# Kernel optimization log

Measured on AMD Instinct MI355X. Metric: run time of the kernel, lower is better.

## Reference

```python
import jax, jax.numpy as jnp
import numpy as np

B, V, H, NT, K_CD = 4096, 1024, 1024, 2, 10
L1_REG, L2_REG = 1e-5, 1e-4


def setup_inputs() -> dict:
    key = jax.random.key(0)
    ks = jax.random.split(key, 10)
    v0 = jax.random.bernoulli(ks[0], 0.5, (B, V)).astype(jnp.float32)
    # two distinct non-trivial (non-Z) sites per sample, one in each half
    tau0 = jax.random.randint(ks[1], (B,), 0, V // 2)
    tau1 = V // 2 + jax.random.randint(ks[2], (B,), 0, V // 2)
    tau_idx = jnp.stack([tau0, tau1], axis=1).astype(jnp.int32)
    basis_choice = jax.random.randint(ks[3], (B, NT), 1, 3).astype(jnp.int32)  # X=1 or Y=2
    basis_ids = jnp.zeros((B, V), jnp.int32)
    basis_ids = basis_ids.at[jnp.arange(B)[:, None], tau_idx].set(basis_choice)
    s = 1.0 / np.sqrt(2.0)
    un = np.zeros((3, 2, 2, 2), np.float32)  # [basis, row, col, re/im]
    un[0, :, :, 0] = np.eye(2)                              # Z: identity
    un[1, :, :, 0] = s * np.array([[1, 1], [1, -1]])        # X: Hadamard
    un[2, :, :, 0] = s * np.array([[1, 0], [1, 0]])         # Y: K gate, real
    un[2, :, :, 1] = s * np.array([[0, -1], [0, 1]])        # Y: K gate, imag
    unitaries = jnp.asarray(un)
    weights_amp = jax.random.normal(ks[4], (H, V), jnp.float32) / np.sqrt(V)
    weights_phase = 0.01 * jax.random.normal(ks[5], (H, V), jnp.float32)
    visible_bias_amp = 0.01 * jax.random.normal(ks[6], (V,), jnp.float32)
    hidden_bias_amp = 0.01 * jax.random.normal(ks[7], (H,), jnp.float32)
    visible_bias_phase = 0.01 * jax.random.normal(ks[8], (V,), jnp.float32)
    hidden_bias_phase = 0.01 * jax.random.normal(ks[9], (H,), jnp.float32)
    return {"v0": v0, "basis_ids": basis_ids, "tau_idx": tau_idx, "unitaries": unitaries,
            "weights_amp": weights_amp, "visible_bias_amp": visible_bias_amp,
            "hidden_bias_amp": hidden_bias_amp, "weights_phase": weights_phase,
            "visible_bias_phase": visible_bias_phase, "hidden_bias_phase": hidden_bias_phase,
            "k": K_CD}


def _forward(v0, unitaries, weights_amp, visible_bias_amp, hidden_bias_amp,
             weights_phase, visible_bias_phase, hidden_bias_phase,
             basis_ids, tau_idx, k):
    Bsz, Vn = v0.shape
    NTn = tau_idx.shape[1]
    C = 2 ** NTn
    # all 2^NT assignments of the rotated (tau) sites -> [C, NT]
    S = jnp.asarray(np.array([[(c >> (NTn - 1 - t)) & 1 for t in range(NTn)]
                              for c in range(C)], np.int32))
    U = (unitaries[..., 0] + 1j * unitaries[..., 1]).astype(jnp.complex64)  # [3,2,2]
    b_tau = jnp.take_along_axis(basis_ids, tau_idx, axis=1)                 # [B,NT]
    v0_tau = jnp.take_along_axis(v0, tau_idx, axis=1).astype(jnp.int32)     # [B,NT]
    # product over tau sites of unitary elements U_b[v0_j, s_j] -> [B,C]
    Uelem = U[b_tau[:, None, :], v0_tau[:, None, :], S[None, :, :]]
    wU = jnp.prod(Uelem, axis=-1)
    # v' = v0 with tau sites replaced by each assignment s -> [B,C,V]
    onehot = jax.nn.one_hot(tau_idx, Vn, dtype=v0.dtype)                    # [B,NT,V]
    mask = onehot.sum(1)
    vp = v0[:, None, :] * (1.0 - mask[:, None, :]) \
         + jnp.einsum('btv,ct->bcv', onehot, S.astype(v0.dtype))
    # unnormalized wavefunction psi(v') = sqrt(p_amp(v')) * exp(i*log(p_phase(v'))/2)
    pre_amp = jnp.einsum('bcv,hv->bch', vp, weights_amp) + hidden_bias_amp
    pre_ph = jnp.einsum('bcv,hv->bch', vp, weights_phase) + hidden_bias_phase
    log_amp = 0.5 * (vp @ visible_bias_amp + jax.nn.softplus(pre_amp).sum(-1))  # [B,C]
    theta = 0.5 * (vp @ visible_bias_phase + jax.nn.softplus(pre_ph).sum(-1))
    # per-sample shift cancels exactly in A/B; keeps exp() in fp32 range
    log_amp = log_amp - jax.lax.stop_gradient(log_amp.max(axis=1, keepdims=True))
    psi = (jnp.exp(log_amp) * (jnp.cos(theta) + 1j * jnp.sin(theta))).astype(jnp.complex64)
    w = wU * psi                                   # [B,C] complex
    coef = w / w.sum(axis=1, keepdims=True)        # A/B weighting per sample
    sig_amp = jax.nn.sigmoid(pre_amp)
    sig_ph = jax.nn.sigmoid(pre_ph)
    inv_b = 1.0 / Bsz
    Lw_amp = jnp.einsum('bc,bch,bcv->hv', coef, sig_amp, vp) * inv_b
    Lw_ph = jnp.einsum('bc,bch,bcv->hv', coef, sig_ph, vp) * inv_b
    Lvb = jnp.einsum('bc,bcv->v', coef, vp) * inv_b
    Lhb_amp = jnp.einsum('bc,bch->h', coef, sig_amp) * inv_b
    Lhb_ph = jnp.einsum('bc,bch->h', coef, sig_ph) * inv_b
    # amplitude params take Re(L) (negated positive phase); phase params take Im(L)
    g_w_amp = -jnp.real(Lw_amp)
    g_vb_amp = -jnp.real(Lvb)
    g_hb_amp = -jnp.real(Lhb_amp)
    g_w_ph = jnp.imag(Lw_ph)
    g_vb_ph = jnp.imag(Lvb)
    g_hb_ph = jnp.imag(Lhb_ph)
    # ---- CD-k Gibbs negative phase (amplitude RBM only) ----
    base_key = jax.random.key(1234)
    def gibbs_step(i, v):
        kh = jax.random.fold_in(base_key, 2 * i)
        kv = jax.random.fold_in(base_key, 2 * i + 1)
        ph = jax.nn.sigmoid(v @ weights_amp.T + hidden_bias_amp)
        h = (jax.random.uniform(kh, ph.shape) < ph).astype(v.dtype)
        pv = jax.nn.sigmoid(h @ weights_amp + visible_bias_amp)
        return (jax.random.uniform(kv, pv.shape) < pv).astype(v.dtype)
    vk = jax.lax.stop_gradient(jax.lax.fori_loop(0, k, gibbs_step, v0))
    sig_k = jax.nn.sigmoid(vk @ weights_amp.T + hidden_bias_amp)
    g_w_amp = g_w_amp + jnp.einsum('bh,bv->hv', sig_k, vk) * inv_b
    g_vb_amp = g_vb_amp + vk.mean(0)
    g_hb_amp = g_hb_amp + sig_k.mean(0)
    # ---- L1/L2 regularization on weight gradients ----
    g_w_amp = g_w_amp + L2_REG * weights_amp + L1_REG * jnp.sign(weights_amp)
    g_w_ph = g_w_ph + L2_REG * weights_phase + L1_REG * jnp.sign(weights_phase)
    return (g_w_amp, g_vb_amp, g_hb_amp, g_w_ph, g_vb_ph, g_hb_ph)


def reference(v0, basis_ids, tau_idx, unitaries, weights_amp, visible_bias_amp,
              hidden_bias_amp, weights_phase, visible_bias_phase, hidden_bias_phase, k):
    return _forward(v0, unitaries, weights_amp, visible_bias_amp, hidden_bias_amp,
                    weights_phase, visible_bias_phase, hidden_bias_phase,
                    basis_ids, tau_idx, k)
```

## Files before the change

kernel.cpp:

```cpp
#include <hip/hip_runtime.h>
#include <cstdint>
#include <cstddef>

#define BSZ 4096
#define VN  1024
#define HN  1024
#define NSTEPS 10

static constexpr float INVB = 1.0f / 4096.0f;
static constexpr float L1R  = 1e-5f;
static constexpr float L2R  = 1e-4f;

typedef __attribute__((ext_vector_type(8)))  __bf16        bf16x8;
typedef __attribute__((ext_vector_type(8)))  unsigned short ushort8;
typedef __attribute__((ext_vector_type(16))) float          f32x16;

__device__ static inline unsigned short f2bf(float x){
  unsigned u = __float_as_uint(x);
  unsigned r = (u + 0x7FFFu + ((u >> 16) & 1u)) >> 16;
  return (unsigned short)r;
}
__device__ static inline float bf2f(unsigned short s){
  return __uint_as_float(((unsigned)s) << 16);
}

__device__ __forceinline__ void gload16(const void* g, void* l){
  __builtin_amdgcn_global_load_lds(
      (__attribute__((address_space(1))) void*)(g),
      (__attribute__((address_space(3))) void*)(l),
      16, 0, 0);
}

#define TFR(x0,x1,r) { x0 += x1; x1 = ((x1)<<(r))|((x1)>>(32-(r))); x1 ^= x0; }

__host__ __device__ static inline void tf2x32(unsigned k0, unsigned k1,
                                              unsigned x0, unsigned x1,
                                              unsigned &o0, unsigned &o1)
{
  const unsigned ks2 = k0 ^ k1 ^ 0x1BD11BDAu;
  x0 += k0; x1 += k1;
  TFR(x0,x1,13) TFR(x0,x1,15) TFR(x0,x1,26) TFR(x0,x1,6)
  x0 += k1; x1 += ks2 + 1u;
  TFR(x0,x1,17) TFR(x0,x1,29) TFR(x0,x1,16) TFR(x0,x1,24)
  x0 += ks2; x1 += k0 + 2u;
  TFR(x0,x1,13) TFR(x0,x1,15) TFR(x0,x1,26) TFR(x0,x1,6)
  x0 += k0; x1 += k1 + 3u;
  TFR(x0,x1,17) TFR(x0,x1,29) TFR(x0,x1,16) TFR(x0,x1,24)
  x0 += k1; x1 += ks2 + 4u;
  TFR(x0,x1,13) TFR(x0,x1,15) TFR(x0,x1,26) TFR(x0,x1,6)
  x0 += ks2; x1 += k0 + 5u;
  o0 = x0; o1 = x1;
}

__device__ static inline float tf_uniform(unsigned k0, unsigned k1, unsigned e)
{
  unsigned o0, o1; tf2x32(k0, k1, 0u, e, o0, o1);
  const unsigned r = o0 ^ o1;
  return __uint_as_float((r >> 9) | 0x3f800000u) - 1.0f;
}

__device__ static inline float sigmoidf(float x){ return 1.0f/(1.0f+expf(-x)); }

__global__ void zero_kernel(float* __restrict__ p, int n){
  int i = blockIdx.x*256 + threadIdx.x;
  if (i < n) p[i] = 0.0f;
}

__global__ void prep_kernel(const float* __restrict__ v0,
                            const int* __restrict__ tau,
                            float* __restrict__ v0m,
                            float* __restrict__ v_cur,
                            unsigned short* __restrict__ v0m_bf,
                            unsigned short* __restrict__ v_bf)
{
  int i = blockIdx.x*256 + threadIdx.x;
  int b = i >> 10;
  int v = i & (VN-1);
  float x = v0[i];
  v_cur[i] = x;
  v_bf[i]  = f2bf(x);
  int t0 = tau[2*b], t1 = tau[2*b+1];
  float xm = (v==t0 || v==t1) ? 0.0f : x;
  v0m[i]    = xm;
  v0m_bf[i] = f2bf(xm);
}

__global__ void transpose_kernel(const float* __restrict__ Wa,
                                 const float* __restrict__ Wp,
                                 float* __restrict__ WTa,
                                 float* __restrict__ WTp)
{
  __shared__ float tile[32][33];
  const float* in = blockIdx.z ? Wp : Wa;
  float* out      = blockIdx.z ? WTp : WTa;
  int x  = blockIdx.x*32 + threadIdx.x;
  int y0 = blockIdx.y*32;
  for (int j = threadIdx.y; j < 32; j += 8)
    tile[j][threadIdx.x] = in[(size_t)(y0+j)*VN + x];
  __syncthreads();
  int xo  = y0 + threadIdx.x;
  int yo0 = blockIdx.x*32;
  for (int j = threadIdx.y; j < 32; j += 8)
    out[(size_t)(yo0+j)*HN + xo] = tile[threadIdx.x][j];
}

__global__ void transpose_to_bf(const float* __restrict__ X,
                                unsigned short* __restrict__ XT)
{
  __shared__ float tile[32][33];
  int x  = blockIdx.x*32 + threadIdx.x;
  int y0 = blockIdx.y*32;
  for (int j = threadIdx.y; j < 32; j += 8)
    tile[j][threadIdx.x] = X[(size_t)(y0+j)*1024 + x];
  __syncthreads();
  int xo  = y0 + threadIdx.x;
  int yo0 = blockIdx.x*32;
  for (int j = threadIdx.y; j < 32; j += 8)
    XT[(size_t)(yo0+j)*BSZ + xo] = f2bf(tile[threadIdx.x][j]);
}

__global__ void split_weights(const float* __restrict__ Wa,
                              const float* __restrict__ Wp,
                              const float* __restrict__ WTa,
                              unsigned short* __restrict__ WaHi,
                              unsigned short* __restrict__ WaLo,
                              unsigned short* __restrict__ WpHi,
                              unsigned short* __restrict__ WpLo,
                              unsigned short* __restrict__ WaTHi,
                              unsigned short* __restrict__ WaTLo)
{
  size_t i = (size_t)blockIdx.x*256 + threadIdx.x;
  float w = Wa[i];  unsigned short h = f2bf(w);
  WaHi[i] = h;  WaLo[i] = f2bf(w - bf2f(h));
  w = Wp[i];  h = f2bf(w);
  WpHi[i] = h;  WpLo[i] = f2bf(w - bf2f(h));
  w = WTa[i]; h = f2bf(w);
  WaTHi[i] = h; WaTLo[i] = f2bf(w - bf2f(h));
}

#define GM 64
#define GN 64
#define GK 64

template<int MODE>
__global__ __launch_bounds__(256) void mfma_nt(
    const unsigned short* __restrict__ A,
    const unsigned short* __restrict__ Bhi,
    const unsigned short* __restrict__ Blo,
    const float* __restrict__ bias,
    unsigned short* __restrict__ out_bf,
    float* __restrict__ out_f,
    unsigned key0, unsigned key1)
{
  constexpr int K = 1024;
  constexpr int N = 1024;
  __shared__ ushort8 ldsA [GM*8];
  __shared__ ushort8 ldsBh[GN*8];
  __shared__ ushort8 ldsBl[GN*8];

  const int orig = blockIdx.x + gridDim.x * blockIdx.y;
  const int swz  = (orig & 7) * 128 + (orig >> 3);
  const int bx   = swz & 15, by = swz >> 4;
  const int m0   = by*GM, n0 = bx*GN;

  const int tid  = threadIdx.x;
  const int lane = tid & 63, w = tid >> 6;
  const int wm = w >> 1, wn = w & 1;
  const int l31 = lane & 31, hi = lane >> 5;
  const int rsub = lane >> 3;
  const int cch  = lane & 7;

  f32x16 acc = {};

  const int arow = wm*32 + l31;
  const int brow = wn*32 + l31;
  const int aswz = arow & 7;
  const int bswz = brow & 7;
  const int aidx = arow*8;
  const int bidx = brow*8;

  for (int kt = 0; kt < K/GK; ++kt){
    __syncthreads();
    const size_t kbase = (size_t)kt*GK;
    #pragma unroll
    for (int p = 0; p < 2; p++){
      const int row  = p*32 + w*8 + rsub;
      const int csrc = cch ^ (row & 7);
      gload16(A   + (size_t)(m0+row)*K + kbase + csrc*8, &ldsA [(p*32 + w*8)*8]);
      gload16(Bhi + (size_t)(n0+row)*K + kbase + csrc*8, &ldsBh[(p*32 + w*8)*8]);
      gload16(Blo + (size_t)(n0+row)*K + kbase + csrc*8, &ldsBl[(p*32 + w*8)*8]);
    }
    __syncthreads();

    #pragma unroll
    for (int s = 0; s < 4; s++){
      const int c = s*2 + hi;
      const bf16x8 a  = __builtin_bit_cast(bf16x8, ldsA [aidx + (c ^ aswz)]);
      const bf16x8 bh = __builtin_bit_cast(bf16x8, ldsBh[bidx + (c ^ bswz)]);
      const bf16x8 bl = __builtin_bit_cast(bf16x8, ldsBl[bidx + (c ^ bswz)]);
      acc = __builtin_amdgcn_mfma_f32_32x32x16_bf16(a, bh, acc, 0, 0, 0);
      acc = __builtin_amdgcn_mfma_f32_32x32x16_bf16(a, bl, acc, 0, 0, 0);
    }
  }

  const int n  = n0 + wn*32 + l31;
  const float bv = bias[n];
  const int mbase = m0 + wm*32 + 4*hi;
  #pragma unroll
  for (int r = 0; r < 16; r++){
    const int m = mbase + (r&3) + 8*(r>>2);
    const float pre = acc[r] + bv;
    const size_t o = (size_t)m*N + n;
    if constexpr (MODE == 0 || MODE == 1){
      const float p = sigmoidf(pre);
      const float u = tf_uniform(key0, key1, (unsigned)(m*N + n));
      out_bf[o] = (u < p) ? (unsigned short)0x3F80 : (unsigned short)0;
      if constexpr (MODE == 1) out_f[o] = (u < p) ? 1.0f : 0.0f;
    } else if constexpr (MODE == 2){
      out_f[o] = sigmoidf(pre);
    } else {
      out_f[o] = pre;
    }
  }
}

template<int NPROD>
__global__ __launch_bounds__(256) void mfma_grad(
    const unsigned short* __restrict__ A1,
    const unsigned short* __restrict__ B1,
    const unsigned short* __restrict__ A2,
    const unsigned short* __restrict__ B2,
    const float* __restrict__ Wreg,
    float* __restrict__ gW)
{
  constexpr int K = BSZ;
  __shared__ ushort8 lA1[64*8];
  __shared__ ushort8 lB1[64*8];
  __shared__ ushort8 lA2[(NPROD==2)?64*8:1];
  __shared__ ushort8 lB2[(NPROD==2)?64*8:1];

  const int tid  = threadIdx.x;
  const int m0   = blockIdx.y*64, n0 = blockIdx.x*64;
  const int lane = tid & 63, w = tid >> 6;
  const int wm = w >> 1, wn = w & 1;
  const int l31 = lane & 31, hi = lane >> 5;
  const int srow = tid >> 3, sc = tid & 7;

  f32x16 acc1a = {}, acc1b = {}, acc2a = {}, acc2b = {};

  const int arow = wm*32 + l31;
  const int brow = wn*32 + l31;
  const int aswz = arow & 7, bswz = brow & 7;
  const int aidx = arow*8,  bidx = brow*8;

  for (int kt = 0; kt < K/64; ++kt){
    __syncthreads();
    const size_t kof = (size_t)kt*64 + sc*8;
    #pragma unroll
    for (int p = 0; p < 2; p++){
      const int row = p*32 + srow;
      const int c = sc ^ (row & 7);
      lA1[row*8 + c] = *(const ushort8*)(A1 + (size_t)(m0+row)*K + kof);
      lB1[row*8 + c] = *(const ushort8*)(B1 + (size_t)(n0+row)*K + kof);
      if constexpr (NPROD==2){
        lA2[row*8 + c] = *(const ushort8*)(A2 + (size_t)(m0+row)*K + kof);
        lB2[row*8 + c] = *(const ushort8*)(B2 + (size_t)(n0+row)*K + kof);
      }
    }
    __syncthreads();
    #pragma unroll
    for (int s = 0; s < 4; s++){
      const int c = s*2 + hi;
      const bf16x8 a1 = __builtin_bit_cast(bf16x8, lA1[aidx + (c ^ aswz)]);
      const bf16x8 b1 = __builtin_bit_cast(bf16x8, lB1[bidx + (c ^ bswz)]);
      if (s & 1) acc1b = __builtin_amdgcn_mfma_f32_32x32x16_bf16(a1, b1, acc1b, 0,0,0);
      else       acc1a = __builtin_amdgcn_mfma_f32_32x32x16_bf16(a1, b1, acc1a, 0,0,0);
      if constexpr (NPROD==2){
        const bf16x8 a2 = __builtin_bit_cast(bf16x8, lA2[aidx + (c ^ aswz)]);
        const bf16x8 b2 = __builtin_bit_cast(bf16x8, lB2[bidx + (c ^ bswz)]);
        if (s & 1) acc2b = __builtin_amdgcn_mfma_f32_32x32x16_bf16(a2, b2, acc2b, 0,0,0);
        else       acc2a = __builtin_amdgcn_mfma_f32_32x32x16_bf16(a2, b2, acc2a, 0,0,0);
      }
    }
  }

  const int n = n0 + wn*32 + l31;
  #pragma unroll
  for (int r = 0; r < 16; r++){
    const int m = m0 + wm*32 + 4*hi + (r&3) + 8*(r>>2);
    const size_t o = (size_t)m*VN + n;
    float val;
    if constexpr (NPROD==2)
      val = INVB*((acc1a[r]+acc1b[r]) - (acc2a[r]+acc2b[r]));
    else
      val = INVB*(acc1a[r]+acc1b[r]);
    const float wv = Wreg[o];
    const float sg = (wv>0.f)?1.f:((wv<0.f)?-1.f:0.f);
    gW[o] += val + L2R*wv + L1R*sg;
  }
}

__global__ __launch_bounds__(256) void coef_ramp_kernel(
    const float* __restrict__ pre0a, const float* __restrict__ pre0p,
    const float* __restrict__ WTa,   const float* __restrict__ WTp,
    const float* __restrict__ v0,
    const float* __restrict__ vbA,   const float* __restrict__ vbP,
    const int*   __restrict__ tau,   const int*   __restrict__ basis,
    const float* __restrict__ unit,
    float* __restrict__ coefRe, float* __restrict__ coefIm,
    float* __restrict__ tmpA,   float* __restrict__ tmpP,
    float* __restrict__ Ramp,   float* __restrict__ Iph)
{
  const int b = blockIdx.x;
  const int t = threadIdx.x;
  const int t0 = tau[2*b], t1 = tau[2*b+1];

  float d[6] = {0,0,0,0,0,0};
  float st_sa[4], st_sp[4], st_a0[4], st_a1[4], st_p0[4], st_p1[4];

  #pragma unroll
  for (int i = 0; i < 4; i++){
    const int h = t + i*256;
    const float pa = pre0a[(size_t)b*HN + h], pp = pre0p[(size_t)b*HN + h];
    const float a0 = WTa[(size_t)t0*HN + h], a1 = WTa[(size_t)t1*HN + h];
    const float p0 = WTp[(size_t)t0*HN + h], p1 = WTp[(size_t)t1*HN + h];
    const float sa  = sigmoidf(pa);
    const float sp  = sigmoidf(pp);
    const float s1a = sa*(1.f-sa), ta2 = 1.f-2.f*sa, s2a = s1a*ta2;
    const float s1p = sp*(1.f-sp), tp2 = 1.f-2.f*sp, s2p = s1p*tp2;
    const float a01 = a0 + a1, p01 = p0 + p1;
    d[0] += a1 *(sa + a1 *(0.5f*s1a + 0.16666667f*a1 *s2a));
    d[1] += a0 *(sa + a0 *(0.5f*s1a + 0.16666667f*a0 *s2a));
    d[2] += a01*(sa + a01*(0.5f*s1a + 0.16666667f*a01*s2a));
    d[3] += p1 *(sp + p1 *(0.5f*s1p + 0.16666667f*p1 *s2p));
    d[4] += p0 *(sp + p0 *(0.5f*s1p + 0.16666667f*p0 *s2p));
    d[5] += p01*(sp + p01*(0.5f*s1p + 0.16666667f*p01*s2p));
    st_sa[i]=sa; st_sp[i]=sp; st_a0[i]=a0; st_a1[i]=a1; st_p0[i]=p0; st_p1[i]=p1;
  }

  __shared__ float red[6][4];
  __shared__ float lcr[4], lci[4];
  const int lane = t & 63, wv = t >> 6;
  #pragma unroll
  for (int i=0;i<6;i++){
    float x = d[i];
    for (int off=32; off>0; off>>=1) x += __shfl_down(x, off);
    if (lane==0) red[i][wv] = x;
  }
  __syncthreads();

  if (t==0){
    double ds[6];
    #pragma unroll
    for (int i=0;i<6;i++)
      ds[i] = (double)red[i][0]+red[i][1]+red[i][2]+red[i][3];

    const int bas0 = basis[(size_t)b*VN + t0], bas1 = basis[(size_t)b*VN + t1];
    const int x0 = (int)v0[(size_t)b*VN + t0], x1 = (int)v0[(size_t)b*VN + t1];
    const double A0 = vbA[t0], A1 = vbA[t1], P0 = vbP[t0], P1 = vbP[t1];

    double la[4], th[4];
    la[0]=0.0;                th[0]=0.0;
    la[1]=0.5*(A1+ds[0]);     th[1]=0.5*(P1+ds[3]);
    la[2]=0.5*(A0+ds[1]);     th[2]=0.5*(P0+ds[4]);
    la[3]=0.5*(A0+A1+ds[2]);  th[3]=0.5*(P0+P1+ds[5]);

    double wR[4], wI[4], sr=0.0, si=0.0;
    #pragma unroll
    for (int c=0;c<4;c++){
      const int s0 = (c>>1)&1, s1 = c&1;
      const float* u0 = unit + (((size_t)bas0*2 + x0)*2 + s0)*2;
      const float* u1 = unit + (((size_t)bas1*2 + x1)*2 + s1)*2;
      const double uR = (double)u0[0]*u1[0] - (double)u0[1]*u1[1];
      const double uI = (double)u0[0]*u1[1] + (double)u0[1]*u1[0];
      const double e  = exp(la[c]);
      const double cs = cos(th[c]), sn = sin(th[c]);
      wR[c] = e*(uR*cs - uI*sn);
      wI[c] = e*(uR*sn + uI*cs);
      sr += wR[c]; si += wI[c];
    }
    const double dd = sr*sr + si*si;
    #pragma unroll
    for (int c=0;c<4;c++){
      const float cr = (float)((wR[c]*sr + wI[c]*si)/dd);
      const float ci = (float)((wI[c]*sr - wR[c]*si)/dd);
      coefRe[b*4+c] = cr;  coefIm[b*4+c] = ci;
      lcr[c] = cr;         lci[c] = ci;
    }
    atomicAdd(tmpA + t0, lcr[2]+lcr[3]);
    atomicAdd(tmpA + t1, lcr[1]+lcr[3]);
    atomicAdd(tmpP + t0, lci[2]+lci[3]);
    atomicAdd(tmpP + t1, lci[1]+lci[3]);
  }
  __syncthreads();

  const float cr0=lcr[0], cr1=lcr[1], cr2=lcr[2], cr3=lcr[3];
  const float ci0=lci[0], ci1=lci[1], ci2=lci[2], ci3=lci[3];

  #pragma unroll
  for (int i = 0; i < 4; i++){
    const int h = t + i*256;
    const float sa = st_sa[i], sp = st_sp[i];
    const float a0 = st_a0[i], a1 = st_a1[i], p0 = st_p0[i], p1 = st_p1[i];
    const float s1a = sa*(1.f-sa), ta2 = 1.f-2.f*sa;
    const float s2a = s1a*ta2,     s3a = s1a*(ta2*ta2 - 2.f*s1a);
    const float s1p = sp*(1.f-sp), tp2 = 1.f-2.f*sp;
    const float s2p = s1p*tp2,     s3p = s1p*(tp2*tp2 - 2.f*s1p);
    const float a01 = a0 + a1, p01 = p0 + p1;
    const float sgA1 = sa + a1 *(s1a + a1 *(0.5f*s2a + 0.16666667f*a1 *s3a));
    const float sgA0 = sa + a0 *(s1a + a0 *(0.5f*s2a + 0.16666667f*a0 *s3a));
    const float sgA01= sa + a01*(s1a + a01*(0.5f*s2a + 0.16666667f*a01*s3a));
    const float sgP1 = sp + p1 *(s1p + p1 *(0.5f*s2p + 0.16666667f*p1 *s3p));
    const float sgP0 = sp + p0 *(s1p + p0 *(0.5f*s2p + 0.16666667f*p0 *s3p));
    const float sgP01= sp + p01*(s1p + p01*(0.5f*s2p + 0.16666667f*p01*s3p));
    Ramp[(size_t)b*HN + h] = cr0*sa + cr1*sgA1 + cr2*sgA0 + cr3*sgA01;
    Iph [(size_t)b*HN + h] = ci0*sp + ci1*sgP1 + ci2*sgP0 + ci3*sgP01;
  }
}

__global__ void csr_count(const int* __restrict__ tau, int* __restrict__ cnt){
  int b = blockIdx.x*256 + threadIdx.x;
  atomicAdd(cnt + tau[2*b],   1);
  atomicAdd(cnt + tau[2*b+1], 1);
}

__global__ __launch_bounds__(1024) void csr_scan(const int* __restrict__ cnt,
                                                 int* __restrict__ off,
                                                 int* __restrict__ cur){
  __shared__ int s[1024];
  const int t = threadIdx.x;
  s[t] = cnt[t];
  __syncthreads();
  for (int d=1; d<1024; d<<=1){
    int v = 0;
    if (t >= d) v = s[t-d];
    __syncthreads();
    s[t] += v;
    __syncthreads();
  }
  const int excl = (t==0) ? 0 : s[t-1];
  off[t] = excl; cur[t] = excl;
}

__global__ void csr_fill(const int* __restrict__ tau, int* __restrict__ cur,
                         int* __restrict__ list){
  int b = blockIdx.x*256 + threadIdx.x;
  int p0 = atomicAdd(cur + tau[2*b],   1); list[p0] = b;
  int p1 = atomicAdd(cur + tau[2*b+1], 1); list[p1] = b;
}

__global__ __launch_bounds__(256) void scatter_v2(
    const float* __restrict__ pre0a, const float* __restrict__ pre0p,
    const float* __restrict__ WTa,   const float* __restrict__ WTp,
    const int*   __restrict__ tau,
    const float* __restrict__ coefRe, const float* __restrict__ coefIm,
    const int* __restrict__ cnt, const int* __restrict__ off,
    const int* __restrict__ list,
    float* __restrict__ gWa, float* __restrict__ gWp)
{
  const int v = blockIdx.x;
  const int n = cnt[v];
  if (n == 0) return;
  const int o = off[v];
  const int c_lo = (v < 512) ? 2 : 1;

  const int h = blockIdx.y*256 + threadIdx.x;
  const float av = WTa[(size_t)v*HN + h];
  const float pv = WTp[(size_t)v*HN + h];
  float accA = 0.f, accP = 0.f;
  for (int e = o; e < o + n; e++){
    const int b = list[e];
    const int t0 = tau[2*b], t1 = tau[2*b+1];
    const int other = (v < 512) ? t1 : t0;
    const float aoA = WTa[(size_t)other*HN + h];
    const float aoP = WTp[(size_t)other*HN + h];
    const float pa  = pre0a[(size_t)b*HN + h];
    const float pp  = pre0p[(size_t)b*HN + h];
    const float crl = coefRe[b*4 + c_lo], cr3 = coefRe[b*4 + 3];
    const float cil = coefIm[b*4 + c_lo], ci3 = coefIm[b*4 + 3];
    accA += crl*sigmoidf(pa + av) + cr3*sigmoidf(pa + av + aoA);
    accP += cil*sigmoidf(pp + pv) + ci3*sigmoidf(pp + pv + aoP);
  }
  gWa[(size_t)h*VN + v] += -INVB*accA;
  gWp[(size_t)h*VN + v] +=  INVB*accP;
}

__global__ __launch_bounds__(256) void colsum_v2(
    const float* __restrict__ v0m, const float* __restrict__ vk,
    const float* __restrict__ sigk, const float* __restrict__ Ramp,
    const float* __restrict__ Iph,
    float* __restrict__ csV0m, float* __restrict__ csVk,
    float* __restrict__ csSigk, float* __restrict__ csRamp,
    float* __restrict__ csIph)
{
  const int j  = blockIdx.x*256 + threadIdx.x;
  const int b0 = blockIdx.y*128;
  float s1=0,s2=0,s3=0,s4=0,s5=0;
  for (int b=b0; b<b0+128; b++){
    const size_t o = (size_t)b*1024 + j;
    s1 += v0m[o]; s2 += vk[o]; s3 += sigk[o]; s4 += Ramp[o]; s5 += Iph[o];
  }
  atomicAdd(csV0m+j, s1); atomicAdd(csVk+j, s2); atomicAdd(csSigk+j, s3);
  atomicAdd(csRamp+j, s4); atomicAdd(csIph+j, s5);
}

__global__ void final_small(
    const float* __restrict__ csV0m, const float* __restrict__ csVk,
    const float* __restrict__ csSigk, const float* __restrict__ csRamp,
    const float* __restrict__ csIph,
    const float* __restrict__ tmpA, const float* __restrict__ tmpP,
    float* __restrict__ gVa, float* __restrict__ gHa,
    float* __restrict__ gVp, float* __restrict__ gHp)
{
  const int j = blockIdx.x*256 + threadIdx.x;
  if (j < VN){
    gVa[j] = INVB*(csVk[j] - csV0m[j] - tmpA[j]);
    gVp[j] = INVB*tmpP[j];
  }
  if (j < HN){
    gHa[j] = INVB*(csSigk[j] - csRamp[j]);
    gHp[j] = INVB*csIph[j];
  }
}

extern "C" void kernel_launch(void* const* d_in, const int* in_sizes, int n_in,
                              void* d_out, int out_size, void* d_ws, size_t ws_size,
                              hipStream_t stream)
{
  const float* v0    = (const float*)d_in[0];
  const int*   basis = (const int*)  d_in[1];
  const int*   tau   = (const int*)  d_in[2];
  const float* unit  = (const float*)d_in[3];
  const float* Wa    = (const float*)d_in[4];
  const float* vbA   = (const float*)d_in[5];
  const float* hbA   = (const float*)d_in[6];
  const float* Wp    = (const float*)d_in[7];
  const float* vbP   = (const float*)d_in[8];
  const float* hbP   = (const float*)d_in[9];

  float* ws    = (float*)d_ws;
  float* v0m   = ws;  ws += (size_t)BSZ*VN;
  float* v_cur = ws;  ws += (size_t)BSZ*VN;
  float* h_buf = ws;  ws += (size_t)BSZ*HN;
  float* WTa   = ws;  ws += (size_t)VN*HN;
  float* WTp   = ws;  ws += (size_t)VN*HN;
  float* pre0a = ws;  ws += (size_t)BSZ*HN;
  float* pre0p = ws;  ws += (size_t)BSZ*HN;
  float* Ramp  = ws;  ws += (size_t)BSZ*HN;
  float* Iph   = ws;  ws += (size_t)BSZ*HN;
  float* coefRe= ws;  ws += (size_t)BSZ*4;
  float* coefIm= ws;  ws += (size_t)BSZ*4;
  float* tmpA  = ws;  ws += VN;
  float* tmpP  = ws;  ws += VN;
  float* csV0m = ws;  ws += VN;
  float* csVk  = ws;  ws += VN;
  float* csSigk= ws;  ws += HN;
  float* csRamp= ws;  ws += HN;
  float* csIph = ws;  ws += HN;
  int*   csrCnt = (int*)ws;  ws += VN;
  int*   csrOff = (int*)ws;  ws += VN;
  int*   csrCur = (int*)ws;  ws += VN;
  int*   csrLst = (int*)ws;  ws += 2*BSZ;
  unsigned short* v_bf    = (unsigned short*)ws;  ws += (size_t)BSZ*VN/2;
  unsigned short* h_bf    = (unsigned short*)ws;  ws += (size_t)BSZ*HN/2;
  unsigned short* v0m_bf  = (unsigned short*)ws;  ws += (size_t)BSZ*VN/2;
  unsigned short* WaHi    = (unsigned short*)ws;  ws += (size_t)HN*VN/2;
  unsigned short* WaLo    = (unsigned short*)ws;  ws += (size_t)HN*VN/2;
  unsigned short* WpHi    = (unsigned short*)ws;  ws += (size_t)HN*VN/2;
  unsigned short* WpLo    = (unsigned short*)ws;  ws += (size_t)HN*VN/2;
  unsigned short* WaTHi   = (unsigned short*)ws;  ws += (size_t)HN*VN/2;
  unsigned short* WaTLo   = (unsigned short*)ws;  ws += (size_t)HN*VN/2;

  float* sig_k = h_buf;
  unsigned short* v0mT  = (unsigned short*)pre0a;
  unsigned short* vkT   = v0mT + (size_t)VN*BSZ;
  unsigned short* RampT = (unsigned short*)pre0p;
  unsigned short* IphT  = RampT + (size_t)HN*BSZ;
  unsigned short* sigkT = (unsigned short*)WTa;

  float* out = (float*)d_out;
  float* gWa = out;
  float* gVa = gWa + (size_t)HN*VN;
  float* gHa = gVa + VN;
  float* gWp = gHa + HN;
  float* gVp = gWp + (size_t)HN*VN;
  float* gHp = gVp + VN;

  const dim3 gemm_grid(VN/GN, BSZ/GM);
  const dim3 tr_grid(1024/32, BSZ/32);
  const dim3 tr_blk(32, 8);

  zero_kernel<<<dim3(40), 256, 0, stream>>>(tmpA, 10*1024);
  zero_kernel<<<dim3((out_size+255)/256), 256, 0, stream>>>(out, out_size);
  prep_kernel<<<dim3(BSZ*VN/256), 256, 0, stream>>>(v0, tau, v0m, v_cur, v0m_bf, v_bf);
  transpose_kernel<<<dim3(VN/32, HN/32, 2), dim3(32,8), 0, stream>>>(Wa, Wp, WTa, WTp);
  split_weights<<<dim3(HN*VN/256), 256, 0, stream>>>(
      Wa, Wp, WTa, WaHi, WaLo, WpHi, WpLo, WaTHi, WaTLo);

  mfma_nt<3><<<gemm_grid, 256, 0, stream>>>(
      v0m_bf, WaHi, WaLo, hbA, nullptr, pre0a, 0u, 0u);
  mfma_nt<3><<<gemm_grid, 256, 0, stream>>>(
      v0m_bf, WpHi, WpLo, hbP, nullptr, pre0p, 0u, 0u);
  coef_ramp_kernel<<<dim3(BSZ), 256, 0, stream>>>(
      pre0a, pre0p, WTa, WTp, v0, vbA, vbP, tau, basis, unit,
      coefRe, coefIm, tmpA, tmpP, Ramp, Iph);

  csr_count<<<dim3(BSZ/256), 256, 0, stream>>>(tau, csrCnt);
  csr_scan <<<dim3(1), 1024, 0, stream>>>(csrCnt, csrOff, csrCur);
  csr_fill <<<dim3(BSZ/256), 256, 0, stream>>>(tau, csrCur, csrLst);
  scatter_v2<<<dim3(VN, 4), 256, 0, stream>>>(
      pre0a, pre0p, WTa, WTp, tau, coefRe, coefIm,
      csrCnt, csrOff, csrLst, gWa, gWp);

  for (int i = 0; i < NSTEPS; i++){
    unsigned kh0, kh1, kv0, kv1;
    tf2x32(0u, 1234u, 0u, (unsigned)(2*i),   kh0, kh1);
    tf2x32(0u, 1234u, 0u, (unsigned)(2*i+1), kv0, kv1);
    mfma_nt<0><<<gemm_grid, 256, 0, stream>>>(
        v_bf, WaHi, WaLo, hbA, h_bf, nullptr, kh0, kh1);
    if (i < NSTEPS-1)
      mfma_nt<0><<<gemm_grid, 256, 0, stream>>>(
          h_bf, WaTHi, WaTLo, vbA, v_bf, nullptr, kv0, kv1);
    else
      mfma_nt<1><<<gemm_grid, 256, 0, stream>>>(
          h_bf, WaTHi, WaTLo, vbA, v_bf, v_cur, kv0, kv1);
  }
  mfma_nt<2><<<gemm_grid, 256, 0, stream>>>(
      v_bf, WaHi, WaLo, hbA, nullptr, sig_k, 0u, 0u);

  colsum_v2<<<dim3(4, 32), 256, 0, stream>>>(
      v0m, v_cur, sig_k, Ramp, Iph, csV0m, csVk, csSigk, csRamp, csIph);
  transpose_to_bf<<<tr_grid, tr_blk, 0, stream>>>(v0m,   v0mT);
  transpose_to_bf<<<tr_grid, tr_blk, 0, stream>>>(v_cur, vkT);
  transpose_to_bf<<<tr_grid, tr_blk, 0, stream>>>(Ramp,  RampT);
  transpose_to_bf<<<tr_grid, tr_blk, 0, stream>>>(Iph,   IphT);
  transpose_to_bf<<<tr_grid, tr_blk, 0, stream>>>(sig_k, sigkT);

  mfma_grad<2><<<dim3(VN/64, HN/64), 256, 0, stream>>>(
      sigkT, vkT, RampT, v0mT, Wa, gWa);
  mfma_grad<1><<<dim3(VN/64, HN/64), 256, 0, stream>>>(
      IphT, v0mT, nullptr, nullptr, Wp, gWp);

  final_small<<<dim3(4), 256, 0, stream>>>(
      csV0m, csVk, csSigk, csRamp, csIph, tmpA, tmpP, gVa, gHa, gVp, gHp);
}
```

Baseline: 987.1 us.

## Double-buffer LDS in GEMM, fuse column sums into transposes, unroll scatter

The NT GEMM kernel now double-buffers its LDS tiles. It prefetches the next K tile with async global loads before computing the current one and uses explicit vmcnt waits and barriers, so load latency overlaps the MFMAs. The separate colsum kernel is removed. Each transpose block now reduces its tile columns and atomically adds them into the column sums, which saves a full re-read of five 4096x1024 arrays. The scatter loop is unrolled by two to expose more memory-level parallelism. Risks are the doubled LDS use, a hand-tuned vmcnt count that must match the number of issued loads, and extra atomics in the transposes.

```diff
diff --git a/kernel.cpp b/kernel.cpp
--- a/kernel.cpp
+++ b/kernel.cpp
@@ -105,18 +105,30 @@
 }
 
 __global__ void transpose_to_bf(const float* __restrict__ X,
-                                unsigned short* __restrict__ XT)
+                                unsigned short* __restrict__ XT,
+                                float* __restrict__ cs)
 {
   __shared__ float tile[32][33];
-  int x  = blockIdx.x*32 + threadIdx.x;
+  const int tx = threadIdx.x, ty = threadIdx.y;
+  int x  = blockIdx.x*32 + tx;
   int y0 = blockIdx.y*32;
-  for (int j = threadIdx.y; j < 32; j += 8)
-    tile[j][threadIdx.x] = X[(size_t)(y0+j)*1024 + x];
+  for (int j = ty; j < 32; j += 8)
+    tile[j][tx] = X[(size_t)(y0+j)*1024 + x];
   __syncthreads();
-  int xo  = y0 + threadIdx.x;
+  int xo  = y0 + tx;
   int yo0 = blockIdx.x*32;
-  for (int j = threadIdx.y; j < 32; j += 8)
-    XT[(size_t)(yo0+j)*BSZ + xo] = f2bf(tile[threadIdx.x][j]);
+  for (int j = ty; j < 32; j += 8)
+    XT[(size_t)(yo0+j)*BSZ + xo] = f2bf(tile[tx][j]);
+  float s = tile[ty][tx] + tile[ty+8][tx] + tile[ty+16][tx] + tile[ty+24][tx];
+  __syncthreads();
+  tile[ty][tx] = s;
+  __syncthreads();
+  if (ty == 0){
+    float t = 0.f;
+    #pragma unroll
+    for (int j = 0; j < 8; j++) t += tile[j][tx];
+    atomicAdd(cs + x, t);
+  }
 }
 
 __global__ void split_weights(const float* __restrict__ Wa,
@@ -154,9 +166,9 @@
 {
   constexpr int K = 1024;
   constexpr int N = 1024;
-  __shared__ ushort8 ldsA [GM*8];
-  __shared__ ushort8 ldsBh[GN*8];
-  __shared__ ushort8 ldsBl[GN*8];
+  __shared__ ushort8 ldsA [2][GM*8];
+  __shared__ ushort8 ldsBh[2][GN*8];
+  __shared__ ushort8 ldsBl[2][GN*8];
 
   const int orig = blockIdx.x + gridDim.x * blockIdx.y;
   const int swz  = (orig & 7) * 128 + (orig >> 3);
@@ -179,28 +191,44 @@
   const int aidx = arow*8;
   const int bidx = brow*8;
 
-  for (int kt = 0; kt < K/GK; ++kt){
-    __syncthreads();
+  auto STAGE = [&](int kt, int buf){
     const size_t kbase = (size_t)kt*GK;
     #pragma unroll
     for (int p = 0; p < 2; p++){
       const int row  = p*32 + w*8 + rsub;
       const int csrc = cch ^ (row & 7);
-      gload16(A   + (size_t)(m0+row)*K + kbase + csrc*8, &ldsA [(p*32 + w*8)*8]);
-      gload16(Bhi + (size_t)(n0+row)*K + kbase + csrc*8, &ldsBh[(p*32 + w*8)*8]);
-      gload16(Blo + (size_t)(n0+row)*K + kbase + csrc*8, &ldsBl[(p*32 + w*8)*8]);
-    }
-    __syncthreads();
+      gload16(A   + (size_t)(m0+row)*K + kbase + csrc*8, &ldsA [buf][(p*32 + w*8)*8]);
+      gload16(Bhi + (size_t)(n0+row)*K + kbase + csrc*8, &ldsBh[buf][(p*32 + w*8)*8]);
+      gload16(Blo + (size_t)(n0+row)*K + kbase + csrc*8, &ldsBl[buf][(p*32 + w*8)*8]);
+    }
+  };
+
+  STAGE(0, 0);
+
+  #pragma unroll 2
+  for (int kt = 0; kt < K/GK; ++kt){
+    const int cur = kt & 1;
+    if (kt + 1 < K/GK){
+      STAGE(kt+1, cur^1);
+      asm volatile("s_waitcnt vmcnt(6)" ::: "memory");
+    } else {
+      asm volatile("s_waitcnt vmcnt(0)" ::: "memory");
+    }
+    __builtin_amdgcn_sched_barrier(0);
+    __builtin_amdgcn_s_barrier();
+    __builtin_amdgcn_sched_barrier(0);
 
     #pragma unroll
     for (int s = 0; s < 4; s++){
       const int c = s*2 + hi;
-      const bf16x8 a  = __builtin_bit_cast(bf16x8, ldsA [aidx + (c ^ aswz)]);
-      const bf16x8 bh = __builtin_bit_cast(bf16x8, ldsBh[bidx + (c ^ bswz)]);
-      const bf16x8 bl = __builtin_bit_cast(bf16x8, ldsBl[bidx + (c ^ bswz)]);
+      const bf16x8 a  = __builtin_bit_cast(bf16x8, ldsA [cur][aidx + (c ^ aswz)]);
+      const bf16x8 bh = __builtin_bit_cast(bf16x8, ldsBh[cur][bidx + (c ^ bswz)]);
+      const bf16x8 bl = __builtin_bit_cast(bf16x8, ldsBl[cur][bidx + (c ^ bswz)]);
       acc = __builtin_amdgcn_mfma_f32_32x32x16_bf16(a, bh, acc, 0, 0, 0);
       acc = __builtin_amdgcn_mfma_f32_32x32x16_bf16(a, bl, acc, 0, 0, 0);
     }
+    __builtin_amdgcn_sched_barrier(0);
+    __builtin_amdgcn_s_barrier();
   }
 
   const int n  = n0 + wn*32 + l31;
@@ -463,45 +491,44 @@
   if (n == 0) return;
   const int o = off[v];
   const int c_lo = (v < 512) ? 2 : 1;
+  const bool lo_half = (v < 512);
 
   const int h = blockIdx.y*256 + threadIdx.x;
   const float av = WTa[(size_t)v*HN + h];
   const float pv = WTp[(size_t)v*HN + h];
   float accA = 0.f, accP = 0.f;
-  for (int e = o; e < o + n; e++){
-    const int b = list[e];
-    const int t0 = tau[2*b], t1 = tau[2*b+1];
-    const int other = (v < 512) ? t1 : t0;
-    const float aoA = WTa[(size_t)other*HN + h];
-    const float aoP = WTp[(size_t)other*HN + h];
-    const float pa  = pre0a[(size_t)b*HN + h];
-    const float pp  = pre0p[(size_t)b*HN + h];
-    const float crl = coefRe[b*4 + c_lo], cr3 = coefRe[b*4 + 3];
-    const float cil = coefIm[b*4 + c_lo], ci3 = coefIm[b*4 + 3];
-    accA += crl*sigmoidf(pa + av) + cr3*sigmoidf(pa + av + aoA);
-    accP += cil*sigmoidf(pp + pv) + ci3*sigmoidf(pp + pv + aoP);
+  int e = o;
+  for (; e + 2 <= o + n; e += 2){
+    const int b0 = list[e], b1 = list[e+1];
+    const int ot0 = lo_half ? tau[2*b0+1] : tau[2*b0];
+    const int ot1 = lo_half ? tau[2*b1+1] : tau[2*b1];
+    const float aoA0 = WTa[(size_t)ot0*HN + h], aoA1 = WTa[(size_t)ot1*HN + h];
+    const float aoP0 = WTp[(size_t)ot0*HN + h], aoP1 = WTp[(size_t)ot1*HN + h];
+    const float pa0 = pre0a[(size_t)b0*HN + h], pa1 = pre0a[(size_t)b1*HN + h];
+    const float pp0 = pre0p[(size_t)b0*HN + h], pp1 = pre0p[(size_t)b1*HN + h];
+    const float crl0 = coefRe[b0*4 + c_lo], cr30 = coefRe[b0*4 + 3];
+    const float cil0 = coefIm[b0*4 + c_lo], ci30 = coefIm[b0*4 + 3];
+    const float crl1 = coefRe[b1*4 + c_lo], cr31 = coefRe[b1*4 + 3];
+    const float cil1 = coefIm[b1*4 + c_lo], ci31 = coefIm[b1*4 + 3];
+    accA += crl0*sigmoidf(pa0 + av) + cr30*sigmoidf(pa0 + av + aoA0);
+    accP += cil0*sigmoidf(pp0 + pv) + ci30*sigmoidf(pp0 + pv + aoP0);
+    accA += crl1*sigmoidf(pa1 + av) + cr31*sigmoidf(pa1 + av + aoA1);
+    accP += cil1*sigmoidf(pp1 + pv) + ci31*sigmoidf(pp1 + pv + aoP1);
+  }
+  if (e < o + n){
+    const int b0 = list[e];
+    const int ot0 = lo_half ? tau[2*b0+1] : tau[2*b0];
+    const float aoA0 = WTa[(size_t)ot0*HN + h];
+    const float aoP0 = WTp[(size_t)ot0*HN + h];
+    const float pa0 = pre0a[(size_t)b0*HN + h];
+    const float pp0 = pre0p[(size_t)b0*HN + h];
+    const float crl0 = coefRe[b0*4 + c_lo], cr30 = coefRe[b0*4 + 3];
+    const float cil0 = coefIm[b0*4 + c_lo], ci30 = coefIm[b0*4 + 3];
+    accA += crl0*sigmoidf(pa0 + av) + cr30*sigmoidf(pa0 + av + aoA0);
+    accP += cil0*sigmoidf(pp0 + pv) + ci30*sigmoidf(pp0 + pv + aoP0);
   }
   gWa[(size_t)h*VN + v] += -INVB*accA;
   gWp[(size_t)h*VN + v] +=  INVB*accP;
-}
-
-__global__ __launch_bounds__(256) void colsum_v2(
-    const float* __restrict__ v0m, const float* __restrict__ vk,
-    const float* __restrict__ sigk, const float* __restrict__ Ramp,
-    const float* __restrict__ Iph,
-    float* __restrict__ csV0m, float* __restrict__ csVk,
-    float* __restrict__ csSigk, float* __restrict__ csRamp,
-    float* __restrict__ csIph)
-{
-  const int j  = blockIdx.x*256 + threadIdx.x;
-  const int b0 = blockIdx.y*128;
-  float s1=0,s2=0,s3=0,s4=0,s5=0;
-  for (int b=b0; b<b0+128; b++){
-    const size_t o = (size_t)b*1024 + j;
-    s1 += v0m[o]; s2 += vk[o]; s3 += sigk[o]; s4 += Ramp[o]; s5 += Iph[o];
-  }
-  atomicAdd(csV0m+j, s1); atomicAdd(csVk+j, s2); atomicAdd(csSigk+j, s3);
-  atomicAdd(csRamp+j, s4); atomicAdd(csIph+j, s5);
 }
 
 __global__ void final_small(
@@ -628,13 +655,11 @@
   mfma_nt<2><<<gemm_grid, 256, 0, stream>>>(
       v_bf, WaHi, WaLo, hbA, nullptr, sig_k, 0u, 0u);
 
-  colsum_v2<<<dim3(4, 32), 256, 0, stream>>>(
-      v0m, v_cur, sig_k, Ramp, Iph, csV0m, csVk, csSigk, csRamp, csIph);
-  transpose_to_bf<<<tr_grid, tr_blk, 0, stream>>>(v0m,   v0mT);
-  transpose_to_bf<<<tr_grid, tr_blk, 0, stream>>>(v_cur, vkT);
-  transpose_to_bf<<<tr_grid, tr_blk, 0, stream>>>(Ramp,  RampT);
-  transpose_to_bf<<<tr_grid, tr_blk, 0, stream>>>(Iph,   IphT);
-  transpose_to_bf<<<tr_grid, tr_blk, 0, stream>>>(sig_k, sigkT);
+  transpose_to_bf<<<tr_grid, tr_blk, 0, stream>>>(v0m,   v0mT,  csV0m);
+  transpose_to_bf<<<tr_grid, tr_blk, 0, stream>>>(v_cur, vkT,   csVk);
+  transpose_to_bf<<<tr_grid, tr_blk, 0, stream>>>(Ramp,  RampT, csRamp);
+  transpose_to_bf<<<tr_grid, tr_blk, 0, stream>>>(Iph,   IphT,  csIph);
+  transpose_to_bf<<<tr_grid, tr_blk, 0, stream>>>(sig_k, sigkT, csSigk);
 
   mfma_grad<2><<<dim3(VN/64, HN/64), 256, 0, stream>>>(
       sigkT, vkT, RampT, v0mT, Wa, gWa);
```

Result: slower. 1.135 ms (+15.0%).
